# Kernel tuning notes

Hardware: AMD Instinct MI355X
Metric: run time of the kernel (lower is better)

## Reference

```python
import jax, jax.numpy as jnp
import numpy as np

B, M, D = 2048, 40, 64          # batch, num fields, embedding dim
HIDDEN = [128, 128, 128]        # CIN layer sizes


def setup_inputs() -> dict:
    key = jax.random.key(0)
    kx, k0, k1, k2 = jax.random.split(key, 4)
    x = jax.random.normal(kx, (B, M, D), dtype=jnp.float32)
    # torch.rand -> uniform [0, 1)
    W0 = jax.random.uniform(k0, (M, M, HIDDEN[0]), dtype=jnp.float32)
    W1 = jax.random.uniform(k1, (M, HIDDEN[0], HIDDEN[1]), dtype=jnp.float32)
    W2 = jax.random.uniform(k2, (M, HIDDEN[1], HIDDEN[2]), dtype=jnp.float32)
    return {"x": x, "W0": W0, "W1": W1, "W2": W2}


def _cin_forward(x, Ws):
    # x: [b, m, d]. Each layer k:
    #   x_next[b, l, d] = sum_{m, h} x0[b, m, d] * x_k[b, h, d] * W_k[m, h, l]
    # which equals the torch 'bil,bjl->bjil' outer product followed by
    # 'bijk,ijl->bkl' + transpose, but expressed as one fused contraction
    # (opt_einsum picks a path avoiding the worst intermediate).
    ps = []
    xk = x  # [b, H_k, d], H_0 = m
    for W in Ws:
        x_next = jnp.einsum('bmd,bhd,mhl->bld', x, xk, W)  # [b, L_k, d]
        ps.append(jnp.sum(x_next, axis=2))                  # [b, L_k]
        xk = x_next
    return jnp.concatenate(ps, axis=1)                      # [b, sum(L_k)]


def reference(x, W0, W1, W2):
    return _cin_forward(x, (W0, W1, W2))
```

## Files before the change

kernel.cpp:

```cpp
#include <hip/hip_runtime.h>
#include <hip/hip_bf16.h>
#include <cstdint>

#define BATCH 2048
#define MF    40
#define DDIM  64
#define LDIM  128
#define ROWS  (BATCH * DDIM)

typedef __attribute__((ext_vector_type(4)))  short    short4_t;
typedef __attribute__((ext_vector_type(8)))  short    short8;
typedef __attribute__((ext_vector_type(8)))  __bf16   bf16x8;
typedef __attribute__((ext_vector_type(2)))  float    floatx2;
typedef __attribute__((ext_vector_type(16))) float    floatx16;


__device__ __forceinline__ unsigned short f32_to_bf16(float f) {
    union { float f; uint32_t u; } v; v.f = f;
    uint32_t u = v.u;
    uint32_t r = (u + 0x7fffu + ((u >> 16) & 1u)) >> 16;
    return (unsigned short)r;
}

__device__ __forceinline__ void barrier_raw() {
    asm volatile("s_barrier" ::: "memory");
}
__device__ __forceinline__ void lgkmwait0() {
    asm volatile("s_waitcnt lgkmcnt(0)" ::: "memory");
}
template <int N> __device__ __forceinline__ void vmwait() {
    if constexpr (N == 0)  asm volatile("s_waitcnt vmcnt(0)"  ::: "memory");
    if constexpr (N == 4)  asm volatile("s_waitcnt vmcnt(4)"  ::: "memory");
    if constexpr (N == 6)  asm volatile("s_waitcnt vmcnt(6)"  ::: "memory");
    if constexpr (N == 10) asm volatile("s_waitcnt vmcnt(10)" ::: "memory");
}

__global__ void k_wprep_all(const float* __restrict__ W0, const float* __restrict__ W1,
                            const float* __restrict__ W2,
                            unsigned short* __restrict__ W0t,
                            unsigned short* __restrict__ W1t,
                            unsigned short* __restrict__ W2t) {
    int bi = blockIdx.x;
    const float* W; unsigned short* Wt; int KK, H;
    if (bi < 640)       { W = W0; Wt = W0t; KK = 4; H = 40; }
    else if (bi < 1920) { bi -= 640;  W = W1; Wt = W1t; KK = 8; H = 128; }
    else                { bi -= 1920; W = W2; Wt = W2t; KK = 8; H = 128; }
    int lane = threadIdx.x;
    int cb = bi & 3;
    int mkk = bi >> 2;
    int kk = mkk % KK, m = mkk / KK;
    int l = cb * 32 + (lane & 31);
    int hbase = kk * 16 + (lane >> 5) * 8;
    unsigned short o[8];
#pragma unroll
    for (int j = 0; j < 8; ++j) {
        int h = hbase + j;
        float v = (h < H) ? __builtin_nontemporal_load(&W[((size_t)m * H + h) * LDIM + l]) : 0.f;
        o[j] = f32_to_bf16(v);
    }
    *(short8*)(Wt + (((size_t)(m * KK + kk) * 4 + cb) * 64 + lane) * 8) = *(const short8*)o;
}

template <int KK>
__device__ __forceinline__ void layer_loop(
    const unsigned short* __restrict__ Wt,
    const float* __restrict__ x, int b,
    int lane, int hf, int r31, int cbg0, int cbg1,
    unsigned short* slabf,
    bf16x8 (&xk)[2][8], floatx16 (&acc)[2][2])
{
    constexpr int UPM  = KK / 4;
    constexpr int NU   = MF * UPM;
    constexpr int GATE = (KK == 8) ? 10 : 6;

    auto stage = [&](int uu) {
        int u = uu < NU ? uu : NU - 1;
        const unsigned short* src = Wt + (size_t)u * 8192;
        const int tid = threadIdx.x;
#pragma unroll
        for (int it = 0; it < 4; ++it) {
            int c = it * 256 + tid;
            __builtin_amdgcn_global_load_lds(
                (const __attribute__((address_space(1))) uint32_t*)(src + (size_t)c * 8),
                (__attribute__((address_space(3))) uint32_t*)(&slabf[(size_t)(u & 3) * 8192 + (size_t)c * 8]),
                16, 0, 0);
        }
    };
    auto ldfrag = [&](int u, int frag, int cb) {
        return __builtin_bit_cast(bf16x8, *(const short8*)(
            &slabf[(size_t)(u & 3) * 8192 + ((size_t)(frag * 4 + cb) * 64 + lane) * 8]));
    };

    acc[0][0] = floatx16{}; acc[0][1] = floatx16{};
    acc[1][0] = floatx16{}; acc[1][1] = floatx16{};

    float z0;
    asm("v_mov_b32 %0, 0" : "=v"(z0));
    floatx16 zc;
#pragma unroll
    for (int i = 0; i < 16; ++i) zc[i] = z0;

    vmwait<0>();
    float s0n, s1n;
    {
        const float* sp = x + ((size_t)b * MF + 0) * DDIM + r31;
        s0n = sp[0];
        s1n = sp[32];
    }
    stage(0); stage(1); stage(2);
    vmwait<4>();
    barrier_raw();

    bf16x8 bbuf[2][2];
#pragma unroll
    for (int p = 0; p < 2; ++p) {
        bbuf[p][0] = ldfrag(0, p, cbg0);
        bbuf[p][1] = ldfrag(0, p, cbg1);
    }

    float s0v = 0.f, s1v = 0.f;

#pragma unroll 1
    for (int m = 0; m < MF; ++m) {
        floatx16 P[2][2];
#pragma unroll
        for (int kk = 0; kk < KK; ++kk) {
            if (kk % 4 == 0) {
                barrier_raw();
                asm volatile("s_setprio 1");
                if (kk == 0) {
                    s0v = s0n; s1v = s1n;
                    const int mn = (m + 1 < MF) ? m + 1 : MF - 1;
                    const float* sp = x + ((size_t)b * MF + mn) * DDIM + r31;
                    s0n = sp[0];
                    s1n = sp[32];
                }
                stage(m * UPM + kk / 4 + 3);
            }
            const int slot = kk & 1;
            P[0][0] = __builtin_amdgcn_mfma_f32_32x32x16_bf16(bbuf[slot][0], xk[0][kk], (kk == 0) ? zc : P[0][0], 0, 0, 0);
            P[1][0] = __builtin_amdgcn_mfma_f32_32x32x16_bf16(bbuf[slot][0], xk[1][kk], (kk == 0) ? zc : P[1][0], 0, 0, 0);
            P[0][1] = __builtin_amdgcn_mfma_f32_32x32x16_bf16(bbuf[slot][1], xk[0][kk], (kk == 0) ? zc : P[0][1], 0, 0, 0);
            P[1][1] = __builtin_amdgcn_mfma_f32_32x32x16_bf16(bbuf[slot][1], xk[1][kk], (kk == 0) ? zc : P[1][1], 0, 0, 0);
            {
                const int j  = kk + 2;
                int mm = m + ((j >= KK) ? 1 : 0);
                if (mm > MF - 1) mm = MF - 1;
                const int jj = (j >= KK) ? (j - KK) : j;
                const int u  = mm * UPM + jj / 4;
                bbuf[slot][0] = ldfrag(u, jj % 4, cbg0);
                bbuf[slot][1] = ldfrag(u, jj % 4, cbg1);
            }
            if (kk % 4 == 3) vmwait<GATE>();
        }
        asm volatile("s_setprio 0");
#pragma unroll
        for (int t = 0; t < 2; ++t) {
            const float sv = (t == 0) ? s0v : s1v;
            floatx2 s2 = {sv, sv};
#pragma unroll
            for (int cbp = 0; cbp < 2; ++cbp) {
                floatx2*       A = (floatx2*)&acc[t][cbp];
                const floatx2* Q = (const floatx2*)&P[t][cbp];
#pragma unroll
                for (int i = 0; i < 8; ++i) A[i] += s2 * Q[i];
            }
        }
    }
}

__global__ __launch_bounds__(256, 2) void k_cin(
    const float* __restrict__ x,
    const unsigned short* __restrict__ W0t,
    const unsigned short* __restrict__ W1t,
    const unsigned short* __restrict__ W2t,
    float* __restrict__ out)
{
    __shared__ unsigned short slab[4][8192];
    unsigned short* slabf = &slab[0][0];

    if ((blockIdx.x >> 8) & 1) {
        asm volatile("s_sleep 15");
    }

    const int tid  = threadIdx.x;
    const int lane = tid & 63, wave = tid >> 6;
    const int hf   = lane >> 5, r31 = lane & 31;
    const int rowhalf = wave >> 1, colhalf = wave & 1;
    const int b = blockIdx.x * 2 + rowhalf;
    const int cbg0 = colhalf * 2, cbg1 = colhalf * 2 + 1;

    bf16x8   xk[2][8];
    floatx16 acc[2][2];

    auto write_ps = [&](int OFF) {
#pragma unroll
        for (int cbp = 0; cbp < 2; ++cbp) {
#pragma unroll
            for (int j = 0; j < 16; ++j) {
                float v = acc[0][cbp][j] + acc[1][cbp][j];
                v += __shfl_xor(v, 16);
                v += __shfl_xor(v, 8);
                v += __shfl_xor(v, 4);
                v += __shfl_xor(v, 2);
                v += __shfl_xor(v, 1);
                if (r31 == 0)
                    out[(size_t)b * 384 + OFF + (colhalf * 2 + cbp) * 32 +
                        (j & 3) + 8 * (j >> 2) + 4 * hf] = v;
            }
        }
    };

    auto exchange = [&]() {
        vmwait<0>();
        barrier_raw();
#pragma unroll
        for (int t = 0; t < 2; ++t)
#pragma unroll
            for (int cbp = 0; cbp < 2; ++cbp)
#pragma unroll
                for (int g = 0; g < 4; ++g) {
                    unsigned short o[4];
#pragma unroll
                    for (int i = 0; i < 4; ++i) o[i] = f32_to_bf16(acc[t][cbp][g * 4 + i]);
                    const int kk  = colhalf * 4 + cbp * 2 + (g >> 1);
                    const int hfr = g & 1;
                    *(short4_t*)(&slabf[(size_t)rowhalf * 8192 +
                        ((size_t)(t * 8 + kk) * 64 + hfr * 32 + r31) * 8 + 4 * hf]) =
                        *(const short4_t*)o;
                }
        lgkmwait0();
        barrier_raw();
#pragma unroll
        for (int t = 0; t < 2; ++t)
#pragma unroll
            for (int kk = 0; kk < 8; ++kk)
                xk[t][kk] = __builtin_bit_cast(bf16x8, *(const short8*)(
                    &slabf[(size_t)rowhalf * 8192 + ((size_t)(t * 8 + kk) * 64 + lane) * 8]));
        lgkmwait0();
        barrier_raw();
    };

#pragma unroll
    for (int t = 0; t < 2; ++t)
#pragma unroll
        for (int kk = 0; kk < 4; ++kk) {
            unsigned short tmp[8];
#pragma unroll
            for (int j = 0; j < 8; ++j) {
                int h = kk * 16 + hf * 8 + j;
                float v = (h < MF) ? x[((size_t)b * MF + h) * DDIM + t * 32 + r31] : 0.f;
                tmp[j] = f32_to_bf16(v);
            }
            xk[t][kk] = __builtin_bit_cast(bf16x8, *(const short8*)tmp);
        }

    layer_loop<4>(W0t, x, b, lane, hf, r31, cbg0, cbg1, slabf, xk, acc);
    write_ps(0);
    exchange();

    layer_loop<8>(W1t, x, b, lane, hf, r31, cbg0, cbg1, slabf, xk, acc);
    write_ps(128);
    exchange();

    layer_loop<8>(W2t, x, b, lane, hf, r31, cbg0, cbg1, slabf, xk, acc);
    write_ps(256);
}

extern "C" void kernel_launch(void* const* d_in, const int* in_sizes, int n_in,
                              void* d_out, int out_size, void* d_ws, size_t ws_size,
                              hipStream_t stream) {
    const float* x  = (const float*)d_in[0];
    const float* W0 = (const float*)d_in[1];
    const float* W1 = (const float*)d_in[2];
    const float* W2 = (const float*)d_in[3];
    float* out = (float*)d_out;

    char* ws = (char*)d_ws;
    size_t off = 0;
    auto alloc = [&](size_t bytes) -> void* {
        void* p = ws + off;
        off += (bytes + 255) & ~(size_t)255;
        return p;
    };
    unsigned short* W0t = (unsigned short*)alloc((size_t)MF * 4 * 2048 * 2);
    unsigned short* W1t = (unsigned short*)alloc((size_t)MF * 8 * 2048 * 2);
    unsigned short* W2t = (unsigned short*)alloc((size_t)MF * 8 * 2048 * 2);

    k_wprep_all<<<3200, 64, 0, stream>>>(W0, W1, W2, W0t, W1t, W2t);
    k_cin<<<ROWS / 128, 256, 0, stream>>>(x, W0t, W1t, W2t, out);
}
```

Measured before the change: 434.3 us.

## Shrink weight staging ring to three LDS slots and raise occupancy to three blocks

Replaces the four-slot LDS ring for weight tiles with a three-slot rotating ring (prefetch distance 2 instead of 3), with wait placement moved to mid-group. The smaller LDS footprint lets launch bounds target three blocks per CU instead of two, and the staggered s_sleep for odd block groups is removed. The zero-initialised accumulator constant trick is replaced with plain zero-initialised P. The shorter prefetch distance risks exposing more global-load latency, in exchange for more resident waves hiding it.

```diff
diff --git a/kernel.cpp b/kernel.cpp
--- a/kernel.cpp
+++ b/kernel.cpp
@@ -30,9 +30,7 @@
 }
 template <int N> __device__ __forceinline__ void vmwait() {
     if constexpr (N == 0)  asm volatile("s_waitcnt vmcnt(0)"  ::: "memory");
-    if constexpr (N == 4)  asm volatile("s_waitcnt vmcnt(4)"  ::: "memory");
     if constexpr (N == 6)  asm volatile("s_waitcnt vmcnt(6)"  ::: "memory");
-    if constexpr (N == 10) asm volatile("s_waitcnt vmcnt(10)" ::: "memory");
 }
 
 __global__ void k_wprep_all(const float* __restrict__ W0, const float* __restrict__ W1,
@@ -71,9 +69,8 @@
 {
     constexpr int UPM  = KK / 4;
     constexpr int NU   = MF * UPM;
-    constexpr int GATE = (KK == 8) ? 10 : 6;
-
-    auto stage = [&](int uu) {
+
+    auto stage = [&](int uu, int sbase) {
         int u = uu < NU ? uu : NU - 1;
         const unsigned short* src = Wt + (size_t)u * 8192;
         const int tid = threadIdx.x;
@@ -82,52 +79,48 @@
             int c = it * 256 + tid;
             __builtin_amdgcn_global_load_lds(
                 (const __attribute__((address_space(1))) uint32_t*)(src + (size_t)c * 8),
-                (__attribute__((address_space(3))) uint32_t*)(&slabf[(size_t)(u & 3) * 8192 + (size_t)c * 8]),
+                (__attribute__((address_space(3))) uint32_t*)(&slabf[(size_t)sbase + (size_t)c * 8]),
                 16, 0, 0);
         }
     };
-    auto ldfrag = [&](int u, int frag, int cb) {
+    auto ldfrag = [&](int sbase, int frag, int cb) {
         return __builtin_bit_cast(bf16x8, *(const short8*)(
-            &slabf[(size_t)(u & 3) * 8192 + ((size_t)(frag * 4 + cb) * 64 + lane) * 8]));
+            &slabf[(size_t)sbase + ((size_t)(frag * 4 + cb) * 64 + lane) * 8]));
     };
 
     acc[0][0] = floatx16{}; acc[0][1] = floatx16{};
     acc[1][0] = floatx16{}; acc[1][1] = floatx16{};
 
-    float z0;
-    asm("v_mov_b32 %0, 0" : "=v"(z0));
-    floatx16 zc;
-#pragma unroll
-    for (int i = 0; i < 16; ++i) zc[i] = z0;
-
-    vmwait<0>();
+    int c0 = 0, c1 = 8192, c2 = 16384;
+
+    stage(0, c0); stage(1, c1);
     float s0n, s1n;
     {
         const float* sp = x + ((size_t)b * MF + 0) * DDIM + r31;
         s0n = sp[0];
         s1n = sp[32];
     }
-    stage(0); stage(1); stage(2);
-    vmwait<4>();
+    vmwait<0>();
     barrier_raw();
 
     bf16x8 bbuf[2][2];
 #pragma unroll
     for (int p = 0; p < 2; ++p) {
-        bbuf[p][0] = ldfrag(0, p, cbg0);
-        bbuf[p][1] = ldfrag(0, p, cbg1);
+        bbuf[p][0] = ldfrag(c0, p, cbg0);
+        bbuf[p][1] = ldfrag(c0, p, cbg1);
     }
 
     float s0v = 0.f, s1v = 0.f;
 
 #pragma unroll 1
     for (int m = 0; m < MF; ++m) {
-        floatx16 P[2][2];
+        floatx16 P[2][2] = {};
 #pragma unroll
         for (int kk = 0; kk < KK; ++kk) {
             if (kk % 4 == 0) {
                 barrier_raw();
                 asm volatile("s_setprio 1");
+                stage(m * UPM + kk / 4 + 2, c2);
                 if (kk == 0) {
                     s0v = s0n; s1v = s1n;
                     const int mn = (m + 1 < MF) ? m + 1 : MF - 1;
@@ -135,23 +128,22 @@
                     s0n = sp[0];
                     s1n = sp[32];
                 }
-                stage(m * UPM + kk / 4 + 3);
             }
             const int slot = kk & 1;
-            P[0][0] = __builtin_amdgcn_mfma_f32_32x32x16_bf16(bbuf[slot][0], xk[0][kk], (kk == 0) ? zc : P[0][0], 0, 0, 0);
-            P[1][0] = __builtin_amdgcn_mfma_f32_32x32x16_bf16(bbuf[slot][0], xk[1][kk], (kk == 0) ? zc : P[1][0], 0, 0, 0);
-            P[0][1] = __builtin_amdgcn_mfma_f32_32x32x16_bf16(bbuf[slot][1], xk[0][kk], (kk == 0) ? zc : P[0][1], 0, 0, 0);
-            P[1][1] = __builtin_amdgcn_mfma_f32_32x32x16_bf16(bbuf[slot][1], xk[1][kk], (kk == 0) ? zc : P[1][1], 0, 0, 0);
+            P[0][0] = __builtin_amdgcn_mfma_f32_32x32x16_bf16(bbuf[slot][0], xk[0][kk], P[0][0], 0, 0, 0);
+            P[1][0] = __builtin_amdgcn_mfma_f32_32x32x16_bf16(bbuf[slot][0], xk[1][kk], P[1][0], 0, 0, 0);
+            P[0][1] = __builtin_amdgcn_mfma_f32_32x32x16_bf16(bbuf[slot][1], xk[0][kk], P[0][1], 0, 0, 0);
+            P[1][1] = __builtin_amdgcn_mfma_f32_32x32x16_bf16(bbuf[slot][1], xk[1][kk], P[1][1], 0, 0, 0);
             {
-                const int j  = kk + 2;
-                int mm = m + ((j >= KK) ? 1 : 0);
-                if (mm > MF - 1) mm = MF - 1;
-                const int jj = (j >= KK) ? (j - KK) : j;
-                const int u  = mm * UPM + jj / 4;
-                bbuf[slot][0] = ldfrag(u, jj % 4, cbg0);
-                bbuf[slot][1] = ldfrag(u, jj % 4, cbg1);
-            }
-            if (kk % 4 == 3) vmwait<GATE>();
+                const int fr = (kk + 2) & 3;
+                const int sb = ((kk & 3) >= 2) ? c1 : c0;
+                bbuf[slot][0] = ldfrag(sb, fr, cbg0);
+                bbuf[slot][1] = ldfrag(sb, fr, cbg1);
+            }
+            if (kk % 4 == 1) vmwait<6>();
+            if (kk % 4 == 3) {
+                int tmp = c0; c0 = c1; c1 = c2; c2 = tmp;
+            }
         }
         asm volatile("s_setprio 0");
 #pragma unroll
@@ -169,19 +161,15 @@
     }
 }
 
-__global__ __launch_bounds__(256, 2) void k_cin(
+__global__ __launch_bounds__(256, 3) void k_cin(
     const float* __restrict__ x,
     const unsigned short* __restrict__ W0t,
     const unsigned short* __restrict__ W1t,
     const unsigned short* __restrict__ W2t,
     float* __restrict__ out)
 {
-    __shared__ unsigned short slab[4][8192];
+    __shared__ unsigned short slab[3][8192];
     unsigned short* slabf = &slab[0][0];
-
-    if ((blockIdx.x >> 8) & 1) {
-        asm volatile("s_sleep 15");
-    }
 
     const int tid  = threadIdx.x;
     const int lane = tid & 63, wave = tid >> 6;
```

Measured after the change: 1.073 ms. 147% more time.
